# Performance work log

Measured on AMD Instinct MI355X. Metric: run time of the kernel, lower is better.

Reference implementation:

```python
import jax, jax.numpy as jnp
import numpy as np
import math

B, N, H = 2, 2048, 256
NUM_HEADS, HEAD_DIM = 8, 32
WIN = 32            # window_size
WIN_LEN = 2 * WIN + 1


def setup_inputs() -> dict:
    key = jax.random.key(0)
    ks = jax.random.split(key, 12)
    s = 0.02
    return {
        "x": jax.random.normal(ks[0], (B, N, 4, H), dtype=jnp.float32),
        "Wq": jax.random.normal(ks[1], (H, H), dtype=jnp.float32) * s,
        "bq": jnp.zeros((H,), jnp.float32),
        "Wk": jax.random.normal(ks[2], (H, H), dtype=jnp.float32) * s,
        "bk": jnp.zeros((H,), jnp.float32),
        "Wv": jax.random.normal(ks[3], (H, H), dtype=jnp.float32) * s,
        "bv": jnp.zeros((H,), jnp.float32),
        "Wo": jax.random.normal(ks[4], (H, 3 * H), dtype=jnp.float32) * s,
        "bo": jnp.zeros((3 * H,), jnp.float32),
        "Wvec": jax.random.normal(ks[5], (H, 2 * H), dtype=jnp.float32) * s,
        "alpha_dot": jnp.float32(1.0),
        "alpha_norm": jnp.float32(1.0),
        "Wg": jax.random.normal(ks[6], (2 * H, H), dtype=jnp.float32) * s,
        "bg": jnp.zeros((H,), jnp.float32),
    }


def reference(x, Wq, bq, Wk, bk, Wv, bv, Wo, bo, Wvec, alpha_dot, alpha_norm, Wg, bg):
    h, d = NUM_HEADS, HEAD_DIM
    scale = 1.0 / math.sqrt(d)

    x_scalar = x[:, :, 0]          # (B,N,H)
    vec = x[:, :, 1:4]             # (B,N,3,H)

    q = (x_scalar @ Wq + bq).reshape(B, N, h, d).transpose(0, 2, 1, 3)  # (B,h,N,d)
    k = (x_scalar @ Wk + bk).reshape(B, N, h, d).transpose(0, 2, 1, 3)
    v = (x_scalar @ Wv + bv).reshape(B, N, h, d).transpose(0, 2, 1, 3)

    vec_proj = vec @ Wvec                                # (B,N,3,2H)
    vec1, vec2 = vec_proj[..., :H], vec_proj[..., H:]
    vec_dot = (vec1 * vec2).sum(axis=-2)                 # (B,N,H)
    vec_norm = jnp.linalg.norm(vec, axis=2)              # (B,N,H)

    # (B,N,3,h,d) -> (B,h,N,3*d)
    vec_flat = vec.reshape(B, N, 3, h, d).transpose(0, 3, 1, 2, 4).reshape(B, h, N, 3 * d)

    # sliding-window attention via padded gather (matches torch unfold semantics)
    BH = B * h
    q_l = q.reshape(BH, N, d)
    k_l = k.reshape(BH, N, d)
    v_l = v.reshape(BH, N, d)
    vec_l = vec_flat.reshape(BH, N, 3 * d)

    pad = ((0, 0), (WIN, WIN), (0, 0))
    k_p = jnp.pad(k_l, pad)
    v_p = jnp.pad(v_l, pad)
    vec_p = jnp.pad(vec_l, pad)

    idx = jnp.arange(N)[:, None] + jnp.arange(WIN_LEN)[None, :]  # (N,WIN_LEN)
    k_win = k_p[:, idx]        # (BH,N,WIN_LEN,d)
    v_win = v_p[:, idx]
    vec_win = vec_p[:, idx]    # (BH,N,WIN_LEN,3d)

    attn_scores = jnp.einsum('bid,biwd->biw', q_l, k_win) * scale
    attn_weights = jax.nn.softmax(attn_scores, axis=-1)  # (BH,N,WIN_LEN)

    x_agg = jnp.einsum('biw,biwd->bid', attn_weights, v_win).reshape(B, h, N, d)
    vec_aggr = jnp.einsum('biw,biwd->bid', attn_weights, vec_win).reshape(B, h, N, 3 * d)

    x_out = x_agg.transpose(0, 2, 1, 3).reshape(B, N, H)
    vec_aggr = vec_aggr.reshape(B, h, N, 3, d).transpose(0, 2, 3, 1, 4).reshape(B, N, 3, H)

    invariants = jnp.concatenate([alpha_dot * vec_dot, alpha_norm * vec_norm], axis=-1)
    gate = jax.nn.sigmoid(invariants @ Wg + bg)[:, :, None, :]   # (B,N,1,H)
    vec_combined = gate * vec_aggr + vec                          # gated add mixing

    o = x_out @ Wo + bo
    o1, o2, o3 = o[..., :H], o[..., H:2 * H], o[..., 2 * H:]
    x_updated = vec_dot * o1 + vec_norm * o2 + o3

    x_final = jnp.concatenate([x_updated[:, :, None], vec_combined], axis=2)  # (B,N,4,H)
    return x_final, attn_weights
```

## Files before the change

kernel.cpp:

```cpp
#include <hip/hip_runtime.h>
#include <math.h>

#define Bc 2
#define Nn 2048
#define Hh 256
#define NH 8
#define Dd 32
#define WIN 32
#define WL 65
#define BN (Bc * Nn)

typedef __attribute__((ext_vector_type(8))) short bf16x8;
typedef __attribute__((ext_vector_type(4))) float f32x4;

__device__ inline short f2bf(float f) {
    union { float f; unsigned u; } v; v.f = f;
    unsigned r = v.u + 0x7fffu + ((v.u >> 16) & 1u);
    return (short)(r >> 16);
}

__global__ __launch_bounds__(256) void castxw_kernel(
    const float* __restrict__ x, const float* __restrict__ alpha_norm,
    const float* __restrict__ Wq, const float* __restrict__ Wk, const float* __restrict__ Wv,
    const float* __restrict__ Wvec, const float* __restrict__ Wg, const float* __restrict__ Wo,
    short* __restrict__ xs_bf, short* __restrict__ vec_bf,
    float* __restrict__ vec_norm, short* __restrict__ inv_bf,
    short* __restrict__ WqkvT, short* __restrict__ WvecT,
    short* __restrict__ WgT, short* __restrict__ WoT) {
    __shared__ float Ts[32][33];
    if (blockIdx.x < 4096) {
        const int idx = blockIdx.x * 256 + threadIdx.x;
        const int bn = idx >> 8, ch = idx & 255;
        const size_t base = (size_t)bn * 1024 + ch;
        const float xs = x[base];
        const float v0 = x[base + 256], v1 = x[base + 512], v2 = x[base + 768];
        xs_bf[(size_t)bn * 256 + ch] = f2bf(xs);
        vec_bf[((size_t)0 * BN + bn) * 256 + ch] = f2bf(v0);
        vec_bf[((size_t)1 * BN + bn) * 256 + ch] = f2bf(v1);
        vec_bf[((size_t)2 * BN + bn) * 256 + ch] = f2bf(v2);
        const float nrm = sqrtf(v0 * v0 + v1 * v1 + v2 * v2);
        vec_norm[(size_t)bn * 256 + ch] = nrm;
        inv_bf[(size_t)bn * 512 + 256 + ch] = f2bf(alpha_norm[0] * nrm);
        return;
    }
    const int t = threadIdx.x;
    const int cc = t & 31, r0 = t >> 5;
    const int id = blockIdx.x - 4096;
    const float* W; int ldw; short* WT; int ldwt; int n0s, k0, n0d;
    if (id < 192) {
        const int tn = id >> 3, tk = id & 7, sel = tn >> 3;
        W = sel == 0 ? Wq : (sel == 1 ? Wk : Wv); ldw = 256;
        n0s = (tn & 7) * 32; k0 = tk * 32; WT = WqkvT; ldwt = 256; n0d = tn * 32;
    } else if (id < 320) {
        const int id2 = id - 192, tn = id2 >> 3, tk = id2 & 7;
        W = Wvec; ldw = 512; n0s = tn * 32; k0 = tk * 32; WT = WvecT; ldwt = 256; n0d = n0s;
    } else if (id < 448) {
        const int id3 = id - 320, tn = id3 >> 4, tk = id3 & 15;
        W = Wg; ldw = 256; n0s = tn * 32; k0 = tk * 32; WT = WgT; ldwt = 512; n0d = n0s;
    } else {
        const int id4 = id - 448, tn = id4 >> 3, tk = id4 & 7;
        W = Wo; ldw = 768; n0s = tn * 32; k0 = tk * 32; WT = WoT; ldwt = 256; n0d = n0s;
    }
#pragma unroll
    for (int p = 0; p < 4; ++p) {
        const int rr = r0 + p * 8;
        Ts[rr][cc] = W[(size_t)(k0 + rr) * ldw + n0s + cc];
    }
    __syncthreads();
#pragma unroll
    for (int p = 0; p < 4; ++p) {
        const int rr = r0 + p * 8;
        WT[(size_t)(n0d + rr) * ldwt + k0 + cc] = f2bf(Ts[cc][rr]);
    }
}

template<int NT>
__device__ inline void gemm_tiles(const short* __restrict__ A, const short* __restrict__ BT,
                                  int K, int row0, int col0,
                                  short* As, short* Bs, f32x4 acc[2][NT]) {
    const int t = threadIdx.x;
    const int lane = t & 63, wid = t >> 6;
    const int wm = wid & 1, wn = wid >> 1;
    const int quad = lane >> 4, lm = lane & 15;
    const int srow = t >> 2, scg = (t & 3) * 8;
#pragma unroll
    for (int mt = 0; mt < 2; ++mt)
#pragma unroll
        for (int nt = 0; nt < NT; ++nt) {
            f32x4 z = {0.f, 0.f, 0.f, 0.f};
            acc[mt][nt] = z;
        }
    bf16x8 pa = *(const bf16x8*)&A[(size_t)(row0 + srow) * K + scg];
    bf16x8 pb[NT / 2];
#pragma unroll
    for (int p = 0; p < NT / 2; ++p) {
        const int idx = t + p * 256;
        pb[p] = *(const bf16x8*)&BT[(size_t)(col0 + (idx >> 2)) * K + (idx & 3) * 8];
    }
    for (int k0 = 0; k0 < K; k0 += 32) {
        *(bf16x8*)&As[srow * 40 + scg] = pa;
#pragma unroll
        for (int p = 0; p < NT / 2; ++p) {
            const int idx = t + p * 256;
            *(bf16x8*)&Bs[(idx >> 2) * 40 + (idx & 3) * 8] = pb[p];
        }
        __syncthreads();
        if (k0 + 32 < K) {
            pa = *(const bf16x8*)&A[(size_t)(row0 + srow) * K + k0 + 32 + scg];
#pragma unroll
            for (int p = 0; p < NT / 2; ++p) {
                const int idx = t + p * 256;
                pb[p] = *(const bf16x8*)&BT[(size_t)(col0 + (idx >> 2)) * K + k0 + 32 + (idx & 3) * 8];
            }
        }
        bf16x8 af[2], bfr[NT];
#pragma unroll
        for (int mt = 0; mt < 2; ++mt)
            af[mt] = *(bf16x8*)&As[(wm * 32 + mt * 16 + lm) * 40 + quad * 8];
#pragma unroll
        for (int nt = 0; nt < NT; ++nt)
            bfr[nt] = *(bf16x8*)&Bs[(wn * NT * 16 + nt * 16 + lm) * 40 + quad * 8];
#pragma unroll
        for (int mt = 0; mt < 2; ++mt)
#pragma unroll
            for (int nt = 0; nt < NT; ++nt)
                acc[mt][nt] = __builtin_amdgcn_mfma_f32_16x16x32_bf16(
                    af[mt], bfr[nt], acc[mt][nt], 0, 0, 0);
        __syncthreads();
    }
}

__global__ __launch_bounds__(256) void gemm_qkv(
    const short* __restrict__ A, const short* __restrict__ BT,
    const float* __restrict__ bq, const float* __restrict__ bk, const float* __restrict__ bv,
    short* __restrict__ Qb, short* __restrict__ Kb, short* __restrict__ Vb) {
    __shared__ short As[64 * 40];
    __shared__ short Bs[128 * 40];
    f32x4 acc[2][4];
    const int row0 = blockIdx.x * 64, col0 = blockIdx.y * 128;
    gemm_tiles<4>(A, BT, 256, row0, col0, As, Bs, acc);
    const int lane = threadIdx.x & 63, wid = threadIdx.x >> 6;
    const int wm = wid & 1, wn = wid >> 1, quad = lane >> 4, lm = lane & 15;
    const int chunk = col0 >> 8;
    short* dst = chunk == 0 ? Qb : (chunk == 1 ? Kb : Vb);
    const float* bias = chunk == 0 ? bq : (chunk == 1 ? bk : bv);
#pragma unroll
    for (int mt = 0; mt < 2; ++mt)
#pragma unroll
        for (int nt = 0; nt < 4; ++nt) {
            const int col = col0 + wn * 64 + nt * 16 + lm;
            const int cm = col & 255;
            const float bb = bias[cm];
#pragma unroll
            for (int r = 0; r < 4; ++r) {
                const int row = row0 + wm * 32 + mt * 16 + quad * 4 + r;
                dst[(size_t)row * 256 + cm] = f2bf(acc[mt][nt][r] + bb);
            }
        }
}

__global__ __launch_bounds__(256) void gemm_vecdot(
    const short* __restrict__ A, const short* __restrict__ BT,
    const float* __restrict__ alpha_dot,
    float* __restrict__ vec_dot, short* __restrict__ inv_bf) {
    __shared__ short As[3][64 * 40];
    __shared__ short Bs[2][32 * 40];
    const int row0 = blockIdx.x * 64, ch0 = blockIdx.y * 32;
    const int t = threadIdx.x, lane = t & 63, wid = t >> 6;
    const int wm = wid & 1, wn = wid >> 1, quad = lane >> 4, lm = lane & 15;
    const int srow = t >> 2, scg = (t & 3) * 8;
    const int bh_ = t >> 7, bc = (t >> 2) & 31, bcg = (t & 3) * 8;
    f32x4 acc[3][2][2];
#pragma unroll
    for (int p = 0; p < 3; ++p)
#pragma unroll
        for (int h = 0; h < 2; ++h)
#pragma unroll
            for (int mt = 0; mt < 2; ++mt) {
                f32x4 z = {0.f, 0.f, 0.f, 0.f};
                acc[p][h][mt] = z;
            }
    bf16x8 pa[3], pb;
#pragma unroll
    for (int p = 0; p < 3; ++p)
        pa[p] = *(const bf16x8*)&A[((size_t)p * BN + row0 + srow) * 256 + scg];
    pb = *(const bf16x8*)&BT[(size_t)(bh_ * 256 + ch0 + bc) * 256 + bcg];
    for (int k0 = 0; k0 < 256; k0 += 32) {
#pragma unroll
        for (int p = 0; p < 3; ++p)
            *(bf16x8*)&As[p][srow * 40 + scg] = pa[p];
        *(bf16x8*)&Bs[bh_][bc * 40 + bcg] = pb;
        __syncthreads();
        if (k0 + 32 < 256) {
#pragma unroll
            for (int p = 0; p < 3; ++p)
                pa[p] = *(const bf16x8*)&A[((size_t)p * BN + row0 + srow) * 256 + k0 + 32 + scg];
            pb = *(const bf16x8*)&BT[(size_t)(bh_ * 256 + ch0 + bc) * 256 + k0 + 32 + bcg];
        }
        bf16x8 af[3][2], bfr[2];
#pragma unroll
        for (int p = 0; p < 3; ++p)
#pragma unroll
            for (int mt = 0; mt < 2; ++mt)
                af[p][mt] = *(bf16x8*)&As[p][(wm * 32 + mt * 16 + lm) * 40 + quad * 8];
#pragma unroll
        for (int h = 0; h < 2; ++h)
            bfr[h] = *(bf16x8*)&Bs[h][(wn * 16 + lm) * 40 + quad * 8];
#pragma unroll
        for (int p = 0; p < 3; ++p)
#pragma unroll
            for (int h = 0; h < 2; ++h)
#pragma unroll
                for (int mt = 0; mt < 2; ++mt)
                    acc[p][h][mt] = __builtin_amdgcn_mfma_f32_16x16x32_bf16(
                        af[p][mt], bfr[h], acc[p][h][mt], 0, 0, 0);
        __syncthreads();
    }
    const float ad = alpha_dot[0];
#pragma unroll
    for (int mt = 0; mt < 2; ++mt) {
        const int col = ch0 + wn * 16 + lm;
#pragma unroll
        for (int r = 0; r < 4; ++r) {
            const int row = row0 + wm * 32 + mt * 16 + quad * 4 + r;
            float dot = 0.f;
#pragma unroll
            for (int p = 0; p < 3; ++p)
                dot = fmaf(acc[p][0][mt][r], acc[p][1][mt][r], dot);
            vec_dot[(size_t)row * 256 + col] = dot;
            inv_bf[(size_t)row * 512 + col] = f2bf(ad * dot);
        }
    }
}

__global__ __launch_bounds__(256) void gemm_gate(
    const short* __restrict__ A, const short* __restrict__ BT,
    const float* __restrict__ bg, float* __restrict__ gate) {
    __shared__ short As[64 * 40];
    __shared__ short Bs[64 * 40];
    f32x4 acc[2][2];
    const int row0 = blockIdx.x * 64, col0 = blockIdx.y * 64;
    gemm_tiles<2>(A, BT, 512, row0, col0, As, Bs, acc);
    const int lane = threadIdx.x & 63, wid = threadIdx.x >> 6;
    const int wm = wid & 1, wn = wid >> 1, quad = lane >> 4, lm = lane & 15;
#pragma unroll
    for (int mt = 0; mt < 2; ++mt)
#pragma unroll
        for (int nt = 0; nt < 2; ++nt) {
            const int col = col0 + wn * 32 + nt * 16 + lm;
            const float bb = bg[col];
#pragma unroll
            for (int r = 0; r < 4; ++r) {
                const int row = row0 + wm * 32 + mt * 16 + quad * 4 + r;
                const float z = acc[mt][nt][r] + bb;
                gate[(size_t)row * 256 + col] = 1.f / (1.f + __expf(-z));
            }
        }
}

__global__ __launch_bounds__(256) void attn_fused(
    const short* __restrict__ Qb, const short* __restrict__ Kb,
    const short* __restrict__ Vb, const short* __restrict__ vec_bf,
    const float* __restrict__ gate, const float* __restrict__ x,
    float* __restrict__ attnw, float* __restrict__ out, short* __restrict__ xout_bf) {
    const int bh = blockIdx.x >> 6, tile = blockIdx.x & 63;
    const int b = bh >> 3, hd = bh & 7;
    const int i0 = tile * 32;
    const int t = threadIdx.x, lane = t & 63, wid = t >> 6;
    const int wm = wid & 1, wn = wid >> 1, quad = lane >> 4, lm = lane & 15;

    __shared__ __align__(16) short Qs[32 * 40];
    __shared__ __align__(16) short Ks[96 * 40];
    __shared__ __align__(16) short Pb[32 * 104];
    __shared__ __align__(16) short St[128 * 104];

    for (int idx = t; idx < 32 * 104 / 2; idx += 256) ((int*)Pb)[idx] = 0;
    if (t < 128) {
        const int row = t >> 2, cg = t & 3;
        *(bf16x8*)&Qs[row * 40 + cg * 8] =
            *(const bf16x8*)&Qb[((size_t)(b * Nn + i0 + row)) * 256 + hd * 32 + cg * 8];
    }
#pragma unroll
    for (int kk = 0; kk < 2; ++kk) {
        const int idx = t + kk * 256;
        if (idx < 384) {
            const int row = idx >> 2, cg = idx & 3;
            const int j = i0 - WIN + row;
            bf16x8 kv = {0, 0, 0, 0, 0, 0, 0, 0};
            if (j >= 0 && j < Nn)
                kv = *(const bf16x8*)&Kb[((size_t)(b * Nn + j)) * 256 + hd * 32 + cg * 8];
            *(bf16x8*)&Ks[row * 40 + cg * 8] = kv;
        }
    }
    {
        const int chunk = t >> 4, j0 = t & 15;
#pragma unroll
        for (int it = 0; it < 6; ++it) {
            const int jr = j0 + it * 16;
            const int j = i0 - WIN + jr;
            bf16x8 val = {0, 0, 0, 0, 0, 0, 0, 0};
            if (j >= 0 && j < Nn) {
                if (chunk < 4)
                    val = *(const bf16x8*)&Vb[((size_t)(b * Nn + j)) * 256 + hd * 32 + chunk * 8];
                else {
                    const int vc = (chunk - 4) >> 2, d0 = ((chunk - 4) & 3) * 8;
                    val = *(const bf16x8*)&vec_bf[((size_t)vc * BN + b * Nn + j) * 256 + hd * 32 + d0];
                }
            }
#pragma unroll
            for (int u = 0; u < 8; ++u) St[(chunk * 8 + u) * 104 + jr] = val[u];
        }
    }
    __syncthreads();

    if (wid < 2) {
        const int il0 = wid * 16;
        const bf16x8 aq = *(bf16x8*)&Qs[(il0 + lm) * 40 + quad * 8];
        f32x4 c[6];
#pragma unroll
        for (int nt = 0; nt < 6; ++nt) {
            const bf16x8 bk = *(bf16x8*)&Ks[(nt * 16 + lm) * 40 + quad * 8];
            f32x4 z = {0.f, 0.f, 0.f, 0.f};
            c[nt] = __builtin_amdgcn_mfma_f32_16x16x32_bf16(aq, bk, z, 0, 0, 0);
        }
        float mx[4] = {-1e30f, -1e30f, -1e30f, -1e30f};
#pragma unroll
        for (int nt = 0; nt < 6; ++nt)
#pragma unroll
            for (int r = 0; r < 4; ++r) {
                const int il = il0 + quad * 4 + r;
                const int w = nt * 16 + lm - il;
                const float v = (w >= 0 && w <= 64)
                    ? c[nt][r] * 0.17677669529663687f : -1e30f;
                c[nt][r] = v;
                mx[r] = fmaxf(mx[r], v);
            }
#pragma unroll
        for (int off = 1; off < 16; off <<= 1)
#pragma unroll
            for (int r = 0; r < 4; ++r) mx[r] = fmaxf(mx[r], __shfl_xor(mx[r], off, 64));
        float sm[4] = {0.f, 0.f, 0.f, 0.f};
#pragma unroll
        for (int nt = 0; nt < 6; ++nt)
#pragma unroll
            for (int r = 0; r < 4; ++r) {
                const int il = il0 + quad * 4 + r;
                const int w = nt * 16 + lm - il;
                const float e = (w >= 0 && w <= 64) ? __expf(c[nt][r] - mx[r]) : 0.f;
                c[nt][r] = e;
                sm[r] += e;
            }
#pragma unroll
        for (int off = 1; off < 16; off <<= 1)
#pragma unroll
            for (int r = 0; r < 4; ++r) sm[r] += __shfl_xor(sm[r], off, 64);
        float inv[4];
#pragma unroll
        for (int r = 0; r < 4; ++r) inv[r] = 1.f / sm[r];
#pragma unroll
        for (int nt = 0; nt < 6; ++nt)
#pragma unroll
            for (int r = 0; r < 4; ++r) {
                const int il = il0 + quad * 4 + r;
                const int jr = nt * 16 + lm;
                const int w = jr - il;
                if (w >= 0 && w <= 64) {
                    const float pw = c[nt][r] * inv[r];
                    attnw[((size_t)bh * Nn + (i0 + il)) * WL + w] = pw;
                    Pb[il * 104 + jr] = f2bf(pw);
                }
            }
    }
    __syncthreads();

    f32x4 acc[4];
#pragma unroll
    for (int nt = 0; nt < 4; ++nt) {
        f32x4 z = {0.f, 0.f, 0.f, 0.f};
        acc[nt] = z;
    }
#pragma unroll
    for (int ks = 0; ks < 3; ++ks) {
        const bf16x8 ap = *(bf16x8*)&Pb[(wm * 16 + lm) * 104 + ks * 32 + quad * 8];
#pragma unroll
        for (int nt = 0; nt < 4; ++nt) {
            const bf16x8 bs = *(bf16x8*)&St[(wn * 64 + nt * 16 + lm) * 104 + ks * 32 + quad * 8];
            acc[nt] = __builtin_amdgcn_mfma_f32_16x16x32_bf16(ap, bs, acc[nt], 0, 0, 0);
        }
    }
#pragma unroll
    for (int nt = 0; nt < 4; ++nt) {
        const int dim = wn * 64 + nt * 16 + lm;
#pragma unroll
        for (int r = 0; r < 4; ++r) {
            const int i = wm * 16 + quad * 4 + r;
            const size_t bn = (size_t)(b * Nn + i0 + i);
            if (dim < 32) {
                xout_bf[bn * 256 + hd * 32 + dim] = f2bf(acc[nt][r]);
            } else {
                const int dm = dim - 32, c = dm >> 5, dd = dm & 31;
                const int ch = hd * 32 + dd;
                const float g = gate[bn * 256 + ch];
                const size_t off = bn * 1024 + (1 + c) * 256 + ch;
                out[off] = fmaf(g, acc[nt][r], x[off]);
            }
        }
    }
}

__global__ __launch_bounds__(256) void gemm_outf(
    const short* __restrict__ A, const short* __restrict__ BT,
    const float* __restrict__ bo,
    const float* __restrict__ vec_dot, const float* __restrict__ vec_norm,
    float* __restrict__ out) {
    __shared__ short As[64 * 40];
    __shared__ short Bs[3][64 * 40];
    const int row0 = blockIdx.x * 64, ch0 = blockIdx.y * 64;
    const int t = threadIdx.x, lane = t & 63, wid = t >> 6;
    const int wm = wid & 1, wn = wid >> 1, quad = lane >> 4, lm = lane & 15;
    const int srow = t >> 2, scg = (t & 3) * 8;
    f32x4 acc[3][2][2];
#pragma unroll
    for (int p = 0; p < 3; ++p)
#pragma unroll
        for (int mt = 0; mt < 2; ++mt)
#pragma unroll
            for (int nt = 0; nt < 2; ++nt) {
                f32x4 z = {0.f, 0.f, 0.f, 0.f};
                acc[p][mt][nt] = z;
            }
    bf16x8 pa, pb[3];
    pa = *(const bf16x8*)&A[(size_t)(row0 + srow) * 256 + scg];
#pragma unroll
    for (int p = 0; p < 3; ++p)
        pb[p] = *(const bf16x8*)&BT[(size_t)(p * 256 + ch0 + srow) * 256 + scg];
    for (int k0 = 0; k0 < 256; k0 += 32) {
        *(bf16x8*)&As[srow * 40 + scg] = pa;
#pragma unroll
        for (int p = 0; p < 3; ++p)
            *(bf16x8*)&Bs[p][srow * 40 + scg] = pb[p];
        __syncthreads();
        if (k0 + 32 < 256) {
            pa = *(const bf16x8*)&A[(size_t)(row0 + srow) * 256 + k0 + 32 + scg];
#pragma unroll
            for (int p = 0; p < 3; ++p)
                pb[p] = *(const bf16x8*)&BT[(size_t)(p * 256 + ch0 + srow) * 256 + k0 + 32 + scg];
        }
        bf16x8 af[2], bfr[3][2];
#pragma unroll
        for (int mt = 0; mt < 2; ++mt)
            af[mt] = *(bf16x8*)&As[(wm * 32 + mt * 16 + lm) * 40 + quad * 8];
#pragma unroll
        for (int p = 0; p < 3; ++p)
#pragma unroll
            for (int nt = 0; nt < 2; ++nt)
                bfr[p][nt] = *(bf16x8*)&Bs[p][(wn * 32 + nt * 16 + lm) * 40 + quad * 8];
#pragma unroll
        for (int p = 0; p < 3; ++p)
#pragma unroll
            for (int mt = 0; mt < 2; ++mt)
#pragma unroll
                for (int nt = 0; nt < 2; ++nt)
                    acc[p][mt][nt] = __builtin_amdgcn_mfma_f32_16x16x32_bf16(
                        af[mt], bfr[p][nt], acc[p][mt][nt], 0, 0, 0);
        __syncthreads();
    }
#pragma unroll
    for (int mt = 0; mt < 2; ++mt)
#pragma unroll
        for (int nt = 0; nt < 2; ++nt) {
            const int col = ch0 + wn * 32 + nt * 16 + lm;
            const float b1 = bo[col], b2 = bo[256 + col], b3 = bo[512 + col];
#pragma unroll
            for (int r = 0; r < 4; ++r) {
                const int row = row0 + wm * 32 + mt * 16 + quad * 4 + r;
                const float o1 = acc[0][mt][nt][r] + b1;
                const float o2 = acc[1][mt][nt][r] + b2;
                const float o3 = acc[2][mt][nt][r] + b3;
                const float vd = vec_dot[(size_t)row * 256 + col];
                const float vn = vec_norm[(size_t)row * 256 + col];
                out[(size_t)row * 1024 + col] = vd * o1 + vn * o2 + o3;
            }
        }
}

extern "C" void kernel_launch(void* const* d_in, const int* in_sizes, int n_in,
                              void* d_out, int out_size, void* d_ws, size_t ws_size,
                              hipStream_t stream) {
    const float* x  = (const float*)d_in[0];
    const float* Wq = (const float*)d_in[1];
    const float* bq = (const float*)d_in[2];
    const float* Wk = (const float*)d_in[3];
    const float* bk = (const float*)d_in[4];
    const float* Wv = (const float*)d_in[5];
    const float* bv = (const float*)d_in[6];
    const float* Wo = (const float*)d_in[7];
    const float* bo = (const float*)d_in[8];
    const float* Wvec = (const float*)d_in[9];
    const float* alpha_dot  = (const float*)d_in[10];
    const float* alpha_norm = (const float*)d_in[11];
    const float* Wg = (const float*)d_in[12];
    const float* bg = (const float*)d_in[13];

    float* ws = (float*)d_ws;
    float* vec_dot  = ws;
    float* vec_norm = ws + 1048576;
    float* gate     = ws + 2097152;
    short* sb = (short*)(ws + 3145728);
    short* xs_bf   = sb;
    short* vec_bf  = sb + 1048576;
    short* inv_bf  = sb + 4194304;
    short* xout_bf = sb + 6291456;
    short* Q_bf    = sb + 7340032;
    short* K_bf    = sb + 8388608;
    short* V_bf    = sb + 9437184;
    short* WqkvT   = sb + 10485760;
    short* WvecT   = sb + 10682368;
    short* WgT     = sb + 10813440;
    short* WoT     = sb + 10944512;

    float* out = (float*)d_out;
    float* attnw = out + (size_t)Bc * Nn * 4 * Hh;

    castxw_kernel<<<4736, 256, 0, stream>>>(x, alpha_norm, Wq, Wk, Wv, Wvec, Wg, Wo,
                                            xs_bf, vec_bf, vec_norm, inv_bf,
                                            WqkvT, WvecT, WgT, WoT);
    gemm_qkv<<<dim3(64, 6), 256, 0, stream>>>(xs_bf, WqkvT, bq, bk, bv, Q_bf, K_bf, V_bf);
    gemm_vecdot<<<dim3(64, 8), 256, 0, stream>>>(vec_bf, WvecT, alpha_dot, vec_dot, inv_bf);
    gemm_gate<<<dim3(64, 4), 256, 0, stream>>>(inv_bf, WgT, bg, gate);
    attn_fused<<<1024, 256, 0, stream>>>(Q_bf, K_bf, V_bf, vec_bf, gate, x,
                                         attnw, out, xout_bf);
    gemm_outf<<<dim3(64, 4), 256, 0, stream>>>(xout_bf, WoT, bo, vec_dot, vec_norm, out);
}
```

Baseline: 146.3 us.

## Fuse x casting, QKV, vecdot and gate GEMMs into one kernel

Removes the separate fp32-to-bf16 cast pass over x. The QKV, vec-projection/dot and gate GEMMs are merged into a single heterogeneous launch: the first 384 blocks do QKV from fp32 x converted in registers, and the other 256 blocks compute norm, vecdot and gate per 16-row tile with the invariants kept in LDS. The attention kernel now loads the vec windows directly from fp32 x, converting them on the fly, and overlaps that staging with the softmax waves. This cuts kernel launches and intermediate global traffic, at the cost of a large LDS footprint and mixed block roles in fused_mid.

```diff
diff --git a/kernel.cpp b/kernel.cpp
--- a/kernel.cpp
+++ b/kernel.cpp
@@ -1,4 +1,5 @@
 #include <hip/hip_runtime.h>
+#include <hip/hip_bf16.h>
 #include <math.h>
 
 #define Bc 2
@@ -19,33 +20,24 @@
     return (short)(r >> 16);
 }
 
-__global__ __launch_bounds__(256) void castxw_kernel(
-    const float* __restrict__ x, const float* __restrict__ alpha_norm,
+__device__ inline bf16x8 cvt8(float4 a, float4 b) {
+    union { __hip_bfloat162 h[4]; bf16x8 v; } u;
+    u.h[0] = __float22bfloat162_rn(make_float2(a.x, a.y));
+    u.h[1] = __float22bfloat162_rn(make_float2(a.z, a.w));
+    u.h[2] = __float22bfloat162_rn(make_float2(b.x, b.y));
+    u.h[3] = __float22bfloat162_rn(make_float2(b.z, b.w));
+    return u.v;
+}
+
+__global__ __launch_bounds__(256) void castw_kernel(
     const float* __restrict__ Wq, const float* __restrict__ Wk, const float* __restrict__ Wv,
     const float* __restrict__ Wvec, const float* __restrict__ Wg, const float* __restrict__ Wo,
-    short* __restrict__ xs_bf, short* __restrict__ vec_bf,
-    float* __restrict__ vec_norm, short* __restrict__ inv_bf,
     short* __restrict__ WqkvT, short* __restrict__ WvecT,
     short* __restrict__ WgT, short* __restrict__ WoT) {
     __shared__ float Ts[32][33];
-    if (blockIdx.x < 4096) {
-        const int idx = blockIdx.x * 256 + threadIdx.x;
-        const int bn = idx >> 8, ch = idx & 255;
-        const size_t base = (size_t)bn * 1024 + ch;
-        const float xs = x[base];
-        const float v0 = x[base + 256], v1 = x[base + 512], v2 = x[base + 768];
-        xs_bf[(size_t)bn * 256 + ch] = f2bf(xs);
-        vec_bf[((size_t)0 * BN + bn) * 256 + ch] = f2bf(v0);
-        vec_bf[((size_t)1 * BN + bn) * 256 + ch] = f2bf(v1);
-        vec_bf[((size_t)2 * BN + bn) * 256 + ch] = f2bf(v2);
-        const float nrm = sqrtf(v0 * v0 + v1 * v1 + v2 * v2);
-        vec_norm[(size_t)bn * 256 + ch] = nrm;
-        inv_bf[(size_t)bn * 512 + 256 + ch] = f2bf(alpha_norm[0] * nrm);
-        return;
-    }
     const int t = threadIdx.x;
     const int cc = t & 31, r0 = t >> 5;
-    const int id = blockIdx.x - 4096;
+    const int id = blockIdx.x;
     const float* W; int ldw; short* WT; int ldwt; int n0s, k0, n0d;
     if (id < 192) {
         const int tn = id >> 3, tk = id & 7, sel = tn >> 3;
@@ -74,193 +66,248 @@
     }
 }
 
-template<int NT>
-__device__ inline void gemm_tiles(const short* __restrict__ A, const short* __restrict__ BT,
-                                  int K, int row0, int col0,
-                                  short* As, short* Bs, f32x4 acc[2][NT]) {
-    const int t = threadIdx.x;
-    const int lane = t & 63, wid = t >> 6;
-    const int wm = wid & 1, wn = wid >> 1;
+__global__ __launch_bounds__(256) void fused_mid(
+    const float* __restrict__ x,
+    const short* __restrict__ WqkvT, const short* __restrict__ WvecT,
+    const short* __restrict__ WgT,
+    const float* __restrict__ bq, const float* __restrict__ bk, const float* __restrict__ bv,
+    const float* __restrict__ alpha_dot, const float* __restrict__ alpha_norm,
+    const float* __restrict__ bg,
+    short* __restrict__ Qb, short* __restrict__ Kb, short* __restrict__ Vb,
+    float* __restrict__ vec_dot, float* __restrict__ vec_norm, float* __restrict__ gate) {
+    __shared__ __align__(16) short lds[31232];
+    const int bid = blockIdx.x;
+    const int t = threadIdx.x, lane = t & 63, wid = t >> 6;
     const int quad = lane >> 4, lm = lane & 15;
-    const int srow = t >> 2, scg = (t & 3) * 8;
-#pragma unroll
-    for (int mt = 0; mt < 2; ++mt)
-#pragma unroll
-        for (int nt = 0; nt < NT; ++nt) {
-            f32x4 z = {0.f, 0.f, 0.f, 0.f};
-            acc[mt][nt] = z;
-        }
-    bf16x8 pa = *(const bf16x8*)&A[(size_t)(row0 + srow) * K + scg];
-    bf16x8 pb[NT / 2];
-#pragma unroll
-    for (int p = 0; p < NT / 2; ++p) {
-        const int idx = t + p * 256;
-        pb[p] = *(const bf16x8*)&BT[(size_t)(col0 + (idx >> 2)) * K + (idx & 3) * 8];
-    }
-    for (int k0 = 0; k0 < K; k0 += 32) {
-        *(bf16x8*)&As[srow * 40 + scg] = pa;
-#pragma unroll
-        for (int p = 0; p < NT / 2; ++p) {
+
+    if (bid < 384) {
+        short* As = lds;
+        short* Bs = lds + 2560;
+        const int rb = bid & 63, cb = bid >> 6;
+        const int row0 = rb * 64, col0 = cb * 128;
+        const int wm = wid & 1, wn = wid >> 1;
+        const int srow = t >> 2, scg = (t & 3) * 8;
+        f32x4 acc[2][4];
+#pragma unroll
+        for (int mt = 0; mt < 2; ++mt)
+#pragma unroll
+            for (int nt = 0; nt < 4; ++nt) {
+                f32x4 z = {0.f, 0.f, 0.f, 0.f};
+                acc[mt][nt] = z;
+            }
+        float4 pa0 = *(const float4*)&x[(size_t)(row0 + srow) * 1024 + scg];
+        float4 pa1 = *(const float4*)&x[(size_t)(row0 + srow) * 1024 + scg + 4];
+        bf16x8 pb[2];
+#pragma unroll
+        for (int p = 0; p < 2; ++p) {
             const int idx = t + p * 256;
-            *(bf16x8*)&Bs[(idx >> 2) * 40 + (idx & 3) * 8] = pb[p];
+            pb[p] = *(const bf16x8*)&WqkvT[(size_t)(col0 + (idx >> 2)) * 256 + (idx & 3) * 8];
+        }
+        for (int k0 = 0; k0 < 256; k0 += 32) {
+            *(bf16x8*)&As[srow * 40 + scg] = cvt8(pa0, pa1);
+#pragma unroll
+            for (int p = 0; p < 2; ++p) {
+                const int idx = t + p * 256;
+                *(bf16x8*)&Bs[(idx >> 2) * 40 + (idx & 3) * 8] = pb[p];
+            }
+            __syncthreads();
+            if (k0 + 32 < 256) {
+                pa0 = *(const float4*)&x[(size_t)(row0 + srow) * 1024 + k0 + 32 + scg];
+                pa1 = *(const float4*)&x[(size_t)(row0 + srow) * 1024 + k0 + 32 + scg + 4];
+#pragma unroll
+                for (int p = 0; p < 2; ++p) {
+                    const int idx = t + p * 256;
+                    pb[p] = *(const bf16x8*)&WqkvT[(size_t)(col0 + (idx >> 2)) * 256 + k0 + 32 + (idx & 3) * 8];
+                }
+            }
+            bf16x8 af[2], bfr[4];
+#pragma unroll
+            for (int mt = 0; mt < 2; ++mt)
+                af[mt] = *(bf16x8*)&As[(wm * 32 + mt * 16 + lm) * 40 + quad * 8];
+#pragma unroll
+            for (int nt = 0; nt < 4; ++nt)
+                bfr[nt] = *(bf16x8*)&Bs[(wn * 64 + nt * 16 + lm) * 40 + quad * 8];
+#pragma unroll
+            for (int mt = 0; mt < 2; ++mt)
+#pragma unroll
+                for (int nt = 0; nt < 4; ++nt)
+                    acc[mt][nt] = __builtin_amdgcn_mfma_f32_16x16x32_bf16(
+                        af[mt], bfr[nt], acc[mt][nt], 0, 0, 0);
+            __syncthreads();
+        }
+        const int chunk = col0 >> 8;
+        short* dst = chunk == 0 ? Qb : (chunk == 1 ? Kb : Vb);
+        const float* bias = chunk == 0 ? bq : (chunk == 1 ? bk : bv);
+#pragma unroll
+        for (int mt = 0; mt < 2; ++mt)
+#pragma unroll
+            for (int nt = 0; nt < 4; ++nt) {
+                const int col = col0 + (wid >> 1) * 64 + nt * 16 + lm;
+                const int cm = col & 255;
+                const float bb = bias[cm];
+#pragma unroll
+                for (int r = 0; r < 4; ++r) {
+                    const int row = row0 + (wid & 1) * 32 + mt * 16 + quad * 4 + r;
+                    dst[(size_t)row * 256 + cm] = f2bf(acc[mt][nt][r] + bb);
+                }
+            }
+        return;
+    }
+
+    short* As    = lds;
+    short* Bs    = lds + 12672;
+    short* inv_s = lds + 22912;
+    const int row0 = (bid - 384) * 16;
+
+#pragma unroll
+    for (int it = 0; it < 6; ++it) {
+        const int idx = t + it * 256;
+        const int p = idx >> 9, rem = idx & 511, row = rem >> 5, kg = rem & 31;
+        const float* src = &x[(size_t)(row0 + row) * 1024 + (1 + p) * 256 + kg * 8];
+        *(bf16x8*)&As[(p * 16 + row) * 264 + kg * 8] =
+            cvt8(*(const float4*)src, *(const float4*)(src + 4));
+    }
+    const float an = alpha_norm[0], ad = alpha_dot[0];
+#pragma unroll
+    for (int it = 0; it < 4; ++it) {
+        const int idx = t + it * 256;
+        const int row = idx >> 6, c4 = idx & 63;
+        const size_t xb = (size_t)(row0 + row) * 1024 + c4 * 4;
+        const float4 v0 = *(const float4*)&x[xb + 256];
+        const float4 v1 = *(const float4*)&x[xb + 512];
+        const float4 v2 = *(const float4*)&x[xb + 768];
+        float4 nr;
+        nr.x = sqrtf(v0.x * v0.x + v1.x * v1.x + v2.x * v2.x);
+        nr.y = sqrtf(v0.y * v0.y + v1.y * v1.y + v2.y * v2.y);
+        nr.z = sqrtf(v0.z * v0.z + v1.z * v1.z + v2.z * v2.z);
+        nr.w = sqrtf(v0.w * v0.w + v1.w * v1.w + v2.w * v2.w);
+        *(float4*)&vec_norm[(size_t)(row0 + row) * 256 + c4 * 4] = nr;
+        short* ip = &inv_s[row * 520 + 256 + c4 * 4];
+        ip[0] = f2bf(an * nr.x); ip[1] = f2bf(an * nr.y);
+        ip[2] = f2bf(an * nr.z); ip[3] = f2bf(an * nr.w);
+    }
+    __syncthreads();
+
+    for (int cg = 0; cg < 2; ++cg) {
+        f32x4 acc[3][2][2];
+#pragma unroll
+        for (int p = 0; p < 3; ++p)
+#pragma unroll
+            for (int h = 0; h < 2; ++h)
+#pragma unroll
+                for (int nt = 0; nt < 2; ++nt) {
+                    f32x4 z = {0.f, 0.f, 0.f, 0.f};
+                    acc[p][h][nt] = z;
+                }
+        bf16x8 pb[4];
+#pragma unroll
+        for (int q = 0; q < 4; ++q) {
+            const int idx = t + q * 256;
+            const int h = idx >> 9, rem = idx & 511, col = rem >> 2, kg = rem & 3;
+            pb[q] = *(const bf16x8*)&WvecT[(size_t)(h * 256 + cg * 128 + col) * 256 + kg * 8];
+        }
+        for (int k0 = 0; k0 < 256; k0 += 32) {
+#pragma unroll
+            for (int q = 0; q < 4; ++q) {
+                const int idx = t + q * 256;
+                const int h = idx >> 9, rem = idx & 511, col = rem >> 2, kg = rem & 3;
+                *(bf16x8*)&Bs[(h * 128 + col) * 40 + kg * 8] = pb[q];
+            }
+            __syncthreads();
+            if (k0 + 32 < 256) {
+#pragma unroll
+                for (int q = 0; q < 4; ++q) {
+                    const int idx = t + q * 256;
+                    const int h = idx >> 9, rem = idx & 511, col = rem >> 2, kg = rem & 3;
+                    pb[q] = *(const bf16x8*)&WvecT[(size_t)(h * 256 + cg * 128 + col) * 256 + k0 + 32 + kg * 8];
+                }
+            }
+            bf16x8 af[3], bfr[2][2];
+#pragma unroll
+            for (int p = 0; p < 3; ++p)
+                af[p] = *(bf16x8*)&As[(p * 16 + lm) * 264 + k0 + quad * 8];
+#pragma unroll
+            for (int h = 0; h < 2; ++h)
+#pragma unroll
+                for (int nt = 0; nt < 2; ++nt)
+                    bfr[h][nt] = *(bf16x8*)&Bs[(h * 128 + wid * 32 + nt * 16 + lm) * 40 + quad * 8];
+#pragma unroll
+            for (int p = 0; p < 3; ++p)
+#pragma unroll
+                for (int h = 0; h < 2; ++h)
+#pragma unroll
+                    for (int nt = 0; nt < 2; ++nt)
+                        acc[p][h][nt] = __builtin_amdgcn_mfma_f32_16x16x32_bf16(
+                            af[p], bfr[h][nt], acc[p][h][nt], 0, 0, 0);
+            __syncthreads();
+        }
+#pragma unroll
+        for (int nt = 0; nt < 2; ++nt) {
+            const int col = cg * 128 + wid * 32 + nt * 16 + lm;
+#pragma unroll
+            for (int r = 0; r < 4; ++r) {
+                const int row = quad * 4 + r;
+                float dot = 0.f;
+#pragma unroll
+                for (int p = 0; p < 3; ++p)
+                    dot = fmaf(acc[p][0][nt][r], acc[p][1][nt][r], dot);
+                vec_dot[(size_t)(row0 + row) * 256 + col] = dot;
+                inv_s[row * 520 + col] = f2bf(ad * dot);
+            }
         }
         __syncthreads();
-        if (k0 + 32 < K) {
-            pa = *(const bf16x8*)&A[(size_t)(row0 + srow) * K + k0 + 32 + scg];
-#pragma unroll
-            for (int p = 0; p < NT / 2; ++p) {
-                const int idx = t + p * 256;
-                pb[p] = *(const bf16x8*)&BT[(size_t)(col0 + (idx >> 2)) * K + k0 + 32 + (idx & 3) * 8];
-            }
-        }
-        bf16x8 af[2], bfr[NT];
-#pragma unroll
-        for (int mt = 0; mt < 2; ++mt)
-            af[mt] = *(bf16x8*)&As[(wm * 32 + mt * 16 + lm) * 40 + quad * 8];
-#pragma unroll
-        for (int nt = 0; nt < NT; ++nt)
-            bfr[nt] = *(bf16x8*)&Bs[(wn * NT * 16 + nt * 16 + lm) * 40 + quad * 8];
-#pragma unroll
-        for (int mt = 0; mt < 2; ++mt)
-#pragma unroll
-            for (int nt = 0; nt < NT; ++nt)
-                acc[mt][nt] = __builtin_amdgcn_mfma_f32_16x16x32_bf16(
-                    af[mt], bfr[nt], acc[mt][nt], 0, 0, 0);
+    }
+
+    f32x4 g[4];
+#pragma unroll
+    for (int nt = 0; nt < 4; ++nt) {
+        f32x4 z = {0.f, 0.f, 0.f, 0.f};
+        g[nt] = z;
+    }
+    bf16x8 pg[4];
+#pragma unroll
+    for (int q = 0; q < 4; ++q) {
+        const int idx = t + q * 256;
+        pg[q] = *(const bf16x8*)&WgT[(size_t)(idx >> 2) * 512 + (idx & 3) * 8];
+    }
+    for (int k0 = 0; k0 < 512; k0 += 32) {
+#pragma unroll
+        for (int q = 0; q < 4; ++q) {
+            const int idx = t + q * 256;
+            *(bf16x8*)&Bs[(idx >> 2) * 40 + (idx & 3) * 8] = pg[q];
+        }
         __syncthreads();
-    }
-}
-
-__global__ __launch_bounds__(256) void gemm_qkv(
-    const short* __restrict__ A, const short* __restrict__ BT,
-    const float* __restrict__ bq, const float* __restrict__ bk, const float* __restrict__ bv,
-    short* __restrict__ Qb, short* __restrict__ Kb, short* __restrict__ Vb) {
-    __shared__ short As[64 * 40];
-    __shared__ short Bs[128 * 40];
-    f32x4 acc[2][4];
-    const int row0 = blockIdx.x * 64, col0 = blockIdx.y * 128;
-    gemm_tiles<4>(A, BT, 256, row0, col0, As, Bs, acc);
-    const int lane = threadIdx.x & 63, wid = threadIdx.x >> 6;
-    const int wm = wid & 1, wn = wid >> 1, quad = lane >> 4, lm = lane & 15;
-    const int chunk = col0 >> 8;
-    short* dst = chunk == 0 ? Qb : (chunk == 1 ? Kb : Vb);
-    const float* bias = chunk == 0 ? bq : (chunk == 1 ? bk : bv);
-#pragma unroll
-    for (int mt = 0; mt < 2; ++mt)
+        if (k0 + 32 < 512) {
+#pragma unroll
+            for (int q = 0; q < 4; ++q) {
+                const int idx = t + q * 256;
+                pg[q] = *(const bf16x8*)&WgT[(size_t)(idx >> 2) * 512 + k0 + 32 + (idx & 3) * 8];
+            }
+        }
+        const bf16x8 ai = *(bf16x8*)&inv_s[lm * 520 + k0 + quad * 8];
 #pragma unroll
         for (int nt = 0; nt < 4; ++nt) {
-            const int col = col0 + wn * 64 + nt * 16 + lm;
-            const int cm = col & 255;
-            const float bb = bias[cm];
-#pragma unroll
-            for (int r = 0; r < 4; ++r) {
-                const int row = row0 + wm * 32 + mt * 16 + quad * 4 + r;
-                dst[(size_t)row * 256 + cm] = f2bf(acc[mt][nt][r] + bb);
-            }
-        }
-}
-
-__global__ __launch_bounds__(256) void gemm_vecdot(
-    const short* __restrict__ A, const short* __restrict__ BT,
-    const float* __restrict__ alpha_dot,
-    float* __restrict__ vec_dot, short* __restrict__ inv_bf) {
-    __shared__ short As[3][64 * 40];
-    __shared__ short Bs[2][32 * 40];
-    const int row0 = blockIdx.x * 64, ch0 = blockIdx.y * 32;
-    const int t = threadIdx.x, lane = t & 63, wid = t >> 6;
-    const int wm = wid & 1, wn = wid >> 1, quad = lane >> 4, lm = lane & 15;
-    const int srow = t >> 2, scg = (t & 3) * 8;
-    const int bh_ = t >> 7, bc = (t >> 2) & 31, bcg = (t & 3) * 8;
-    f32x4 acc[3][2][2];
-#pragma unroll
-    for (int p = 0; p < 3; ++p)
-#pragma unroll
-        for (int h = 0; h < 2; ++h)
-#pragma unroll
-            for (int mt = 0; mt < 2; ++mt) {
-                f32x4 z = {0.f, 0.f, 0.f, 0.f};
-                acc[p][h][mt] = z;
-            }
-    bf16x8 pa[3], pb;
-#pragma unroll
-    for (int p = 0; p < 3; ++p)
-        pa[p] = *(const bf16x8*)&A[((size_t)p * BN + row0 + srow) * 256 + scg];
-    pb = *(const bf16x8*)&BT[(size_t)(bh_ * 256 + ch0 + bc) * 256 + bcg];
-    for (int k0 = 0; k0 < 256; k0 += 32) {
-#pragma unroll
-        for (int p = 0; p < 3; ++p)
-            *(bf16x8*)&As[p][srow * 40 + scg] = pa[p];
-        *(bf16x8*)&Bs[bh_][bc * 40 + bcg] = pb;
+            const bf16x8 bgf = *(bf16x8*)&Bs[(wid * 64 + nt * 16 + lm) * 40 + quad * 8];
+            g[nt] = __builtin_amdgcn_mfma_f32_16x16x32_bf16(ai, bgf, g[nt], 0, 0, 0);
+        }
         __syncthreads();
-        if (k0 + 32 < 256) {
-#pragma unroll
-            for (int p = 0; p < 3; ++p)
-                pa[p] = *(const bf16x8*)&A[((size_t)p * BN + row0 + srow) * 256 + k0 + 32 + scg];
-            pb = *(const bf16x8*)&BT[(size_t)(bh_ * 256 + ch0 + bc) * 256 + k0 + 32 + bcg];
-        }
-        bf16x8 af[3][2], bfr[2];
-#pragma unroll
-        for (int p = 0; p < 3; ++p)
-#pragma unroll
-            for (int mt = 0; mt < 2; ++mt)
-                af[p][mt] = *(bf16x8*)&As[p][(wm * 32 + mt * 16 + lm) * 40 + quad * 8];
-#pragma unroll
-        for (int h = 0; h < 2; ++h)
-            bfr[h] = *(bf16x8*)&Bs[h][(wn * 16 + lm) * 40 + quad * 8];
-#pragma unroll
-        for (int p = 0; p < 3; ++p)
-#pragma unroll
-            for (int h = 0; h < 2; ++h)
-#pragma unroll
-                for (int mt = 0; mt < 2; ++mt)
-                    acc[p][h][mt] = __builtin_amdgcn_mfma_f32_16x16x32_bf16(
-                        af[p][mt], bfr[h], acc[p][h][mt], 0, 0, 0);
-        __syncthreads();
-    }
-    const float ad = alpha_dot[0];
-#pragma unroll
-    for (int mt = 0; mt < 2; ++mt) {
-        const int col = ch0 + wn * 16 + lm;
+    }
+#pragma unroll
+    for (int nt = 0; nt < 4; ++nt) {
+        const int col = wid * 64 + nt * 16 + lm;
+        const float bb = bg[col];
 #pragma unroll
         for (int r = 0; r < 4; ++r) {
-            const int row = row0 + wm * 32 + mt * 16 + quad * 4 + r;
-            float dot = 0.f;
-#pragma unroll
-            for (int p = 0; p < 3; ++p)
-                dot = fmaf(acc[p][0][mt][r], acc[p][1][mt][r], dot);
-            vec_dot[(size_t)row * 256 + col] = dot;
-            inv_bf[(size_t)row * 512 + col] = f2bf(ad * dot);
-        }
-    }
-}
-
-__global__ __launch_bounds__(256) void gemm_gate(
-    const short* __restrict__ A, const short* __restrict__ BT,
-    const float* __restrict__ bg, float* __restrict__ gate) {
-    __shared__ short As[64 * 40];
-    __shared__ short Bs[64 * 40];
-    f32x4 acc[2][2];
-    const int row0 = blockIdx.x * 64, col0 = blockIdx.y * 64;
-    gemm_tiles<2>(A, BT, 512, row0, col0, As, Bs, acc);
-    const int lane = threadIdx.x & 63, wid = threadIdx.x >> 6;
-    const int wm = wid & 1, wn = wid >> 1, quad = lane >> 4, lm = lane & 15;
-#pragma unroll
-    for (int mt = 0; mt < 2; ++mt)
-#pragma unroll
-        for (int nt = 0; nt < 2; ++nt) {
-            const int col = col0 + wn * 32 + nt * 16 + lm;
-            const float bb = bg[col];
-#pragma unroll
-            for (int r = 0; r < 4; ++r) {
-                const int row = row0 + wm * 32 + mt * 16 + quad * 4 + r;
-                const float z = acc[mt][nt][r] + bb;
-                gate[(size_t)row * 256 + col] = 1.f / (1.f + __expf(-z));
-            }
-        }
+            const int row = row0 + quad * 4 + r;
+            const float z = g[nt][r] + bb;
+            gate[(size_t)row * 256 + col] = 1.f / (1.f + __expf(-z));
+        }
+    }
 }
 
 __global__ __launch_bounds__(256) void attn_fused(
     const short* __restrict__ Qb, const short* __restrict__ Kb,
-    const short* __restrict__ Vb, const short* __restrict__ vec_bf,
+    const short* __restrict__ Vb,
     const float* __restrict__ gate, const float* __restrict__ x,
     float* __restrict__ attnw, float* __restrict__ out, short* __restrict__ xout_bf) {
     const int bh = blockIdx.x >> 6, tile = blockIdx.x & 63;
@@ -292,25 +339,6 @@
             *(bf16x8*)&Ks[row * 40 + cg * 8] = kv;
         }
     }
-    {
-        const int chunk = t >> 4, j0 = t & 15;
-#pragma unroll
-        for (int it = 0; it < 6; ++it) {
-            const int jr = j0 + it * 16;
-            const int j = i0 - WIN + jr;
-            bf16x8 val = {0, 0, 0, 0, 0, 0, 0, 0};
-            if (j >= 0 && j < Nn) {
-                if (chunk < 4)
-                    val = *(const bf16x8*)&Vb[((size_t)(b * Nn + j)) * 256 + hd * 32 + chunk * 8];
-                else {
-                    const int vc = (chunk - 4) >> 2, d0 = ((chunk - 4) & 3) * 8;
-                    val = *(const bf16x8*)&vec_bf[((size_t)vc * BN + b * Nn + j) * 256 + hd * 32 + d0];
-                }
-            }
-#pragma unroll
-            for (int u = 0; u < 8; ++u) St[(chunk * 8 + u) * 104 + jr] = val[u];
-        }
-    }
     __syncthreads();
 
     if (wid < 2) {
@@ -370,6 +398,26 @@
                     Pb[il * 104 + jr] = f2bf(pw);
                 }
             }
+    } else {
+        const int tt = t - 128;
+        const int chunk = tt >> 3, j0 = tt & 7;
+#pragma unroll
+        for (int it = 0; it < 12; ++it) {
+            const int jr = j0 + it * 8;
+            const int j = i0 - WIN + jr;
+            bf16x8 val = {0, 0, 0, 0, 0, 0, 0, 0};
+            if (j >= 0 && j < Nn) {
+                if (chunk < 4) {
+                    val = *(const bf16x8*)&Vb[((size_t)(b * Nn + j)) * 256 + hd * 32 + chunk * 8];
+                } else {
+                    const int vc = (chunk - 4) >> 2, d0 = ((chunk - 4) & 3) * 8;
+                    const float* src = &x[((size_t)(b * Nn + j)) * 1024 + (1 + vc) * 256 + hd * 32 + d0];
+                    val = cvt8(*(const float4*)src, *(const float4*)(src + 4));
+                }
+            }
+#pragma unroll
+            for (int u = 0; u < 8; ++u) St[(chunk * 8 + u) * 104 + jr] = val[u];
+        }
     }
     __syncthreads();
 
@@ -507,28 +555,24 @@
     float* vec_norm = ws + 1048576;
     float* gate     = ws + 2097152;
     short* sb = (short*)(ws + 3145728);
-    short* xs_bf   = sb;
-    short* vec_bf  = sb + 1048576;
-    short* inv_bf  = sb + 4194304;
-    short* xout_bf = sb + 6291456;
-    short* Q_bf    = sb + 7340032;
-    short* K_bf    = sb + 8388608;
-    short* V_bf    = sb + 9437184;
-    short* WqkvT   = sb + 10485760;
-    short* WvecT   = sb + 10682368;
-    short* WgT     = sb + 10813440;
-    short* WoT     = sb + 10944512;
+    short* xout_bf = sb;
+    short* Q_bf    = sb + 1048576;
+    short* K_bf    = sb + 2097152;
+    short* V_bf    = sb + 3145728;
+    short* WqkvT   = sb + 4194304;
+    short* WvecT   = sb + 4390912;
+    short* WgT     = sb + 4521984;
+    short* WoT     = sb + 4653056;
 
     float* out = (float*)d_out;
     float* attnw = out + (size_t)Bc * Nn * 4 * Hh;
 
-    castxw_kernel<<<4736, 256, 0, stream>>>(x, alpha_norm, Wq, Wk, Wv, Wvec, Wg, Wo,
-                                            xs_bf, vec_bf, vec_norm, inv_bf,
-                                            WqkvT, WvecT, WgT, WoT);
-    gemm_qkv<<<dim3(64, 6), 256, 0, stream>>>(xs_bf, WqkvT, bq, bk, bv, Q_bf, K_bf, V_bf);
-    gemm_vecdot<<<dim3(64, 8), 256, 0, stream>>>(vec_bf, WvecT, alpha_dot, vec_dot, inv_bf);
-    gemm_gate<<<dim3(64, 4), 256, 0, stream>>>(inv_bf, WgT, bg, gate);
-    attn_fused<<<1024, 256, 0, stream>>>(Q_bf, K_bf, V_bf, vec_bf, gate, x,
+    castw_kernel<<<640, 256, 0, stream>>>(Wq, Wk, Wv, Wvec, Wg, Wo,
+                                          WqkvT, WvecT, WgT, WoT);
+    fused_mid<<<640, 256, 0, stream>>>(x, WqkvT, WvecT, WgT, bq, bk, bv,
+                                       alpha_dot, alpha_norm, bg,
+                                       Q_bf, K_bf, V_bf, vec_dot, vec_norm, gate);
+    attn_fused<<<1024, 256, 0, stream>>>(Q_bf, K_bf, V_bf, gate, x,
                                          attnw, out, xout_bf);
     gemm_outf<<<dim3(64, 4), 256, 0, stream>>>(xout_bf, WoT, bo, vec_dot, vec_norm, out);
 }
```

After: 154.8 us. 1.06x slower.
